# Kernel optimization log

Measured on AMD Instinct MI355X. Metric: run time of the kernel, lower is better.

## Reference

```python
import jax, jax.numpy as jnp
import numpy as np

B, T, DIM, H = 4, 2048, 512, 8
DECAY = 0.9

def setup_inputs():
    key = jax.random.key(0)
    ks = jax.random.split(key, 8)
    s = 1.0 / np.sqrt(DIM)
    def lin(k):
        return jax.random.normal(k, (DIM, DIM), jnp.float32) * s
    return {
        "q": jax.random.normal(ks[0], (B, T, DIM), jnp.float32),
        "k": jax.random.normal(ks[1], (B, T, DIM), jnp.float32),
        "v": jax.random.normal(ks[2], (B, T, DIM), jnp.float32),
        "Wa": lin(ks[3]), "ba": jnp.zeros((DIM,), jnp.float32),
        "Wb": lin(ks[4]), "bb": jnp.zeros((DIM,), jnp.float32),
        "Wg": lin(ks[5]), "bg": jnp.zeros((DIM,), jnp.float32),
        "Wo": lin(ks[6]), "bo": jnp.zeros((DIM,), jnp.float32),
    }

def _linear_scan(a, b):
    # h_t = a_t * h_{t-1} + b_t along time axis=1, via associative scan
    def combine(c1, c2):
        a1, b1 = c1
        a2, b2 = c2
        return a1 * a2, a2 * b1 + b2
    return jax.lax.associative_scan(combine, (a, b), axis=1)[1]

def reference(q, k, v, Wa, ba, Wb, bb, Wg, bg, Wo, bo):
    # --- Mamba-style selective scan on q (no residual) ---
    a = jax.nn.sigmoid(q @ Wa + ba)   # input-dependent decay [B,T,D]
    b = q @ Wb + bb                   # input injection       [B,T,D]
    h = _linear_scan(a, b)            # recurrent state       [B,T,D]
    g = jax.nn.sigmoid(q @ Wg + bg)   # gate
    m_out = (h * g) @ Wo + bo         # [B,T,D]

    # --- RetNet-style decay-weighted linear retention ---
    Dh = DIM // H
    qh = q.reshape(B, T, H, Dh)
    kh = k.reshape(B, T, H, Dh)
    vh = v.reshape(B, T, H, Dh)
    t = jnp.arange(T)
    delta = t[:, None] - t[None, :]           # t - s
    mask = delta >= 0                         # causal
    decay_mat = jnp.where(
        mask,
        jnp.exp(jnp.where(mask, delta, 0).astype(jnp.float32) * np.float32(np.log(DECAY))),
        0.0,
    )                                          # [T,T]
    scores = jnp.einsum('bthd,bshd->bhts', qh, kh) * decay_mat  # [B,H,T,T]
    r_out = jnp.einsum('bhts,bshd->bthd', scores, vh).reshape(B, T, DIM)

    return m_out + r_out
```

## Files before the change

kernel.cpp:

```cpp
#include <hip/hip_runtime.h>
#include <hip/hip_bf16.h>

typedef unsigned short u16;

#define BB 4
#define TT 2048
#define DIM 512
#define NH 8
#define DH 64
#define DECAY 0.9f

#define CC 64
#define NC 32
#define BHN 32

#define CHS 32
#define NSC 64

#define TM 128
#define TN 128
#define BK 64

#define SS 72

typedef __attribute__((ext_vector_type(8))) short bf16x8;
typedef __attribute__((ext_vector_type(4))) float f32x4;

__device__ __forceinline__ u16 f2bfu(float f) {
  union { float f; unsigned int u; } c; c.f = f;
  unsigned int u = c.u + 0x7FFFu + ((c.u >> 16) & 1u);
  return (u16)(u >> 16);
}
__device__ __forceinline__ float bf2f(u16 u) {
  union { unsigned int u; float f; } c; c.u = ((unsigned int)u) << 16;
  return c.f;
}

__device__ __forceinline__ void gl_lds16(const void* g, void* l) {
  __builtin_amdgcn_global_load_lds(
      (const __attribute__((address_space(1))) void*)g,
      (__attribute__((address_space(3))) void*)(unsigned int)(unsigned long long)l,
      16, 0, 0);
}

__device__ __forceinline__ void gemm_tile(
    int nTile, int mTile, const u16* __restrict__ A, const u16* __restrict__ Bt,
    const float* __restrict__ b0, const float* __restrict__ b1,
    const float* __restrict__ b2,
    u16* __restrict__ C0, u16* __restrict__ C1, u16* __restrict__ C2,
    int act_mask, u16* As, u16* Bs, int tid) {
  int wave = tid >> 6, lane = tid & 63;
  int group = (nTile * TN) >> 9;
  const float* bias = (group == 0) ? b0 : (group == 1) ? b1 : b2;
  u16* C = (group == 0) ? C0 : (group == 1) ? C1 : C2;
  int act = (act_mask >> group) & 1;

  int wm = (wave >> 1) * 64, wn = (wave & 1) * 64;
  int rowA = lane & 15, khalf = lane >> 4;

  f32x4 acc[4][4];
#pragma unroll
  for (int i = 0; i < 4; ++i)
#pragma unroll
    for (int j = 0; j < 4; ++j) acc[i][j] = (f32x4){0.f, 0.f, 0.f, 0.f};

  const u16* Abase = A + (size_t)mTile * TM * 512;
  const u16* Bbase = Bt + (size_t)nTile * TN * 512;

  for (int kk = 0; kk < 512; kk += BK) {
#pragma unroll
    for (int i = 0; i < 4; ++i) {
      int o = (wave * 4 + i) * 64 + lane;
      int row = o >> 3, gk = (o & 7) ^ (row & 7);
      gl_lds16(Abase + (size_t)row * 512 + kk + gk * 8, &As[o * 8]);
    }
#pragma unroll
    for (int i = 0; i < 4; ++i) {
      int o = (wave * 4 + i) * 64 + lane;
      int row = o >> 3, gk = (o & 7) ^ (row & 7);
      gl_lds16(Bbase + (size_t)row * 512 + kk + gk * 8, &Bs[o * 8]);
    }
    __syncthreads();
#pragma unroll
    for (int k0 = 0; k0 < 2; ++k0) {
      bf16x8 af[4], bfr[4];
#pragma unroll
      for (int mi = 0; mi < 4; ++mi) {
        int rr = wm + mi * 16 + rowA;
        int gk = k0 * 4 + khalf;
        int o = rr * 8 + (gk ^ (rr & 7));
        af[mi] = *(const bf16x8*)&As[o * 8];
      }
#pragma unroll
      for (int ni = 0; ni < 4; ++ni) {
        int rr = wn + ni * 16 + rowA;
        int gk = k0 * 4 + khalf;
        int o = rr * 8 + (gk ^ (rr & 7));
        bfr[ni] = *(const bf16x8*)&Bs[o * 8];
      }
#pragma unroll
      for (int mi = 0; mi < 4; ++mi)
#pragma unroll
        for (int ni = 0; ni < 4; ++ni)
          acc[mi][ni] = __builtin_amdgcn_mfma_f32_16x16x32_bf16(
              af[mi], bfr[ni], acc[mi][ni], 0, 0, 0);
    }
    __syncthreads();
  }
  int cloc = lane & 15, rq = (lane >> 4) * 4;
#pragma unroll
  for (int mi = 0; mi < 4; ++mi) {
#pragma unroll
    for (int r = 0; r < 4; ++r) {
      int m = mTile * TM + wm + mi * 16 + rq + r;
#pragma unroll
      for (int ni = 0; ni < 4; ++ni) {
        int n = (nTile * TN + wn + ni * 16 + cloc) & 511;
        float vv = acc[mi][ni][r] + bias[n];
        if (act) vv = 1.0f / (1.0f + __expf(-vv));
        C[(size_t)m * 512 + n] = f2bfu(vv);
      }
    }
  }
}

__device__ __forceinline__ void gemm_tile64(
    int nTile, int mTile, const u16* __restrict__ A, const u16* __restrict__ Bt,
    const float* __restrict__ bias, float* __restrict__ C,
    const u16* __restrict__ Radd, u16* As, u16* Bs, int tid) {
  int wave = tid >> 6, lane = tid & 63;
  int wm = wave * 32;
  int rowA = lane & 15, khalf = lane >> 4;

  f32x4 acc[2][4];
#pragma unroll
  for (int i = 0; i < 2; ++i)
#pragma unroll
    for (int j = 0; j < 4; ++j) acc[i][j] = (f32x4){0.f, 0.f, 0.f, 0.f};

  const u16* Abase = A + (size_t)mTile * TM * 512;
  const u16* Bbase = Bt + (size_t)nTile * 64 * 512;

  for (int kk = 0; kk < 512; kk += BK) {
#pragma unroll
    for (int i = 0; i < 4; ++i) {
      int o = (wave * 4 + i) * 64 + lane;
      int row = o >> 3, gk = (o & 7) ^ (row & 7);
      gl_lds16(Abase + (size_t)row * 512 + kk + gk * 8, &As[o * 8]);
    }
#pragma unroll
    for (int i = 0; i < 2; ++i) {
      int o = (wave * 2 + i) * 64 + lane;
      int row = o >> 3, gk = (o & 7) ^ (row & 7);
      gl_lds16(Bbase + (size_t)row * 512 + kk + gk * 8, &Bs[o * 8]);
    }
    __syncthreads();
#pragma unroll
    for (int k0 = 0; k0 < 2; ++k0) {
      bf16x8 af[2], bfr[4];
#pragma unroll
      for (int mi = 0; mi < 2; ++mi) {
        int rr = wm + mi * 16 + rowA;
        int gk = k0 * 4 + khalf;
        int o = rr * 8 + (gk ^ (rr & 7));
        af[mi] = *(const bf16x8*)&As[o * 8];
      }
#pragma unroll
      for (int ni = 0; ni < 4; ++ni) {
        int rr = ni * 16 + rowA;
        int gk = k0 * 4 + khalf;
        int o = rr * 8 + (gk ^ (rr & 7));
        bfr[ni] = *(const bf16x8*)&Bs[o * 8];
      }
#pragma unroll
      for (int mi = 0; mi < 2; ++mi)
#pragma unroll
        for (int ni = 0; ni < 4; ++ni)
          acc[mi][ni] = __builtin_amdgcn_mfma_f32_16x16x32_bf16(
              af[mi], bfr[ni], acc[mi][ni], 0, 0, 0);
    }
    __syncthreads();
  }
  int cloc = lane & 15, rq = (lane >> 4) * 4;
#pragma unroll
  for (int mi = 0; mi < 2; ++mi) {
#pragma unroll
    for (int r = 0; r < 4; ++r) {
      int m = mTile * TM + wm + mi * 16 + rq + r;
#pragma unroll
      for (int ni = 0; ni < 4; ++ni) {
        int n = nTile * 64 + ni * 16 + cloc;
        float vv = acc[mi][ni][r] + bias[n] + bf2f(Radd[(size_t)m * 512 + n]);
        C[(size_t)m * 512 + n] = vv;
      }
    }
  }
}

__device__ __forceinline__ void dev_retscan(int unit, int tid,
    const u16* __restrict__ KVTb, u16* __restrict__ Ptb) {
  int gid = unit * 256 + tid;
  int bh = gid >> 12, ed = gid & 4095;
  float carry = 0.f;
  const float dC = __powf(DECAY, (float)CC);
#pragma unroll
  for (int c = 0; c < NC; ++c) {
    size_t idx = ((size_t)(c * BHN + bh)) * 4096 + ed;
    Ptb[idx] = f2bfu(carry);
    carry = fmaf(dC, carry, bf2f(KVTb[idx]));
  }
}

__device__ __forceinline__ void dev_part(int unit, int tid,
    const u16* __restrict__ Ab16, const u16* __restrict__ Bb16,
    float2* __restrict__ SAB) {
  int ci = unit >> 3, grp = unit & 7;
  int ch = grp * 256 + tid;
  int bb2 = ch >> 9, d = ch & 511;
  size_t base = ((size_t)bb2 * TT + ci * CHS) * DIM + d;
  float h = 0.f, pA = 1.f;
#pragma unroll
  for (int t = 0; t < CHS; ++t) {
    float av = bf2f(Ab16[base + (size_t)t * DIM]);
    float bv = bf2f(Bb16[base + (size_t)t * DIM]);
    h = fmaf(av, h, bv);
    pA *= av;
  }
  SAB[(size_t)ci * 2048 + ch] = make_float2(pA, h);
}

__device__ __forceinline__ void dev_apply(int unit, int tid,
    const u16* __restrict__ Ab16, const u16* __restrict__ Bb16,
    const u16* __restrict__ g, const float2* __restrict__ SAB,
    u16* __restrict__ hg) {
  int ci = unit >> 3, grp = unit & 7;
  int ch = grp * 256 + tid;
  int bb = ch >> 9, d = ch & 511;
  float carry = 0.f;
  int p = 0;
  for (; p + 8 <= ci; p += 8) {
    float2 s[8];
#pragma unroll
    for (int j = 0; j < 8; ++j) s[j] = SAB[(size_t)(p + j) * 2048 + ch];
#pragma unroll
    for (int j = 0; j < 8; ++j) carry = fmaf(s[j].x, carry, s[j].y);
  }
  for (; p < ci; ++p) {
    float2 s = SAB[(size_t)p * 2048 + ch];
    carry = fmaf(s.x, carry, s.y);
  }
  size_t base = ((size_t)bb * TT + ci * CHS) * DIM + d;
  float h = carry;
#pragma unroll
  for (int t = 0; t < CHS; ++t) {
    size_t idx = base + (size_t)t * DIM;
    h = fmaf(bf2f(Ab16[idx]), h, bf2f(Bb16[idx]));
    hg[idx] = f2bfu(h * bf2f(g[idx]));
  }
}

__device__ __forceinline__ void dev_retout(int unit, int tid,
    u16* Sa, float* dp, float* dpi,
    const u16* __restrict__ qbf, const u16* __restrict__ kcb,
    const u16* __restrict__ VTg, const u16* __restrict__ Ptb,
    u16* __restrict__ routb) {
  int bh = unit & 31, c = unit >> 5;
  int b = bh >> 3, h = bh & 7;
  int wave = tid >> 6, lane = tid & 63;
  size_t base = ((size_t)(b * TT + c * CC)) * DIM + h * DH;
  if (tid < 66) dp[tid] = __powf(DECAY, (float)tid);
  if (tid < 64) dpi[tid] = __powf(DECAY, (float)tid - 63.0f);

  int wm = (wave >> 1) * 32, wn = (wave & 1) * 32;
  int rowA = lane & 15, khalf = lane >> 4;

  bf16x8 afq[2][2];
#pragma unroll
  for (int k0 = 0; k0 < 2; ++k0)
#pragma unroll
    for (int mi = 0; mi < 2; ++mi)
      afq[k0][mi] = *(const bf16x8*)(qbf + base +
          (size_t)(wm + mi * 16 + rowA) * 512 + (k0 * 4 + khalf) * 8);
  const u16* kcbase = kcb + ((size_t)bh * NC + c) * 64 * 64;
  bf16x8 bfk[2][2];
#pragma unroll
  for (int k0 = 0; k0 < 2; ++k0)
#pragma unroll
    for (int ni = 0; ni < 2; ++ni)
      bfk[k0][ni] = *(const bf16x8*)(kcbase +
          (size_t)(wn + ni * 16 + rowA) * 64 + (k0 * 4 + khalf) * 8);

  f32x4 accS[2][2];
#pragma unroll
  for (int i = 0; i < 2; ++i)
#pragma unroll
    for (int j = 0; j < 2; ++j) accS[i][j] = (f32x4){0.f, 0.f, 0.f, 0.f};
#pragma unroll
  for (int k0 = 0; k0 < 2; ++k0)
#pragma unroll
    for (int mi = 0; mi < 2; ++mi)
#pragma unroll
      for (int ni = 0; ni < 2; ++ni)
        accS[mi][ni] = __builtin_amdgcn_mfma_f32_16x16x32_bf16(
            afq[k0][mi], bfk[k0][ni], accS[mi][ni], 0, 0, 0);
  __syncthreads();

  int cloc = lane & 15, rq = (lane >> 4) * 4;
#pragma unroll
  for (int mi = 0; mi < 2; ++mi)
#pragma unroll
    for (int ni = 0; ni < 2; ++ni)
#pragma unroll
      for (int r = 0; r < 4; ++r) {
        int i = wm + mi * 16 + rq + r;
        int j = wn + ni * 16 + cloc;
        float sv = (j <= i) ? accS[mi][ni][r] * dpi[i] : 0.f;
        Sa[i * SS + j] = f2bfu(sv);
      }
#pragma unroll
  for (int mi = 0; mi < 2; ++mi) {
    float s = dp[wm + mi * 16 + rowA + 1];
#pragma unroll
    for (int k0 = 0; k0 < 2; ++k0) {
      bf16x8 t = afq[k0][mi];
#pragma unroll
      for (int u = 0; u < 8; ++u)
        t[u] = (short)f2bfu(bf2f((u16)t[u]) * s);
      afq[k0][mi] = t;
    }
  }
  __syncthreads();

  f32x4 accO[2][2];
#pragma unroll
  for (int i = 0; i < 2; ++i)
#pragma unroll
    for (int j = 0; j < 2; ++j) accO[i][j] = (f32x4){0.f, 0.f, 0.f, 0.f};
#pragma unroll
  for (int k0 = 0; k0 < 4; ++k0) {
    bf16x8 af[2], bfv[2];
#pragma unroll
    for (int mi = 0; mi < 2; ++mi) {
      if (k0 < 2)
        af[mi] = *(const bf16x8*)&Sa[(wm + mi * 16 + rowA) * SS +
                                     (k0 * 4 + khalf) * 8];
      else
        af[mi] = afq[k0 - 2][mi];
    }
#pragma unroll
    for (int ni = 0; ni < 2; ++ni) {
      int e = wn + ni * 16 + rowA;
      if (k0 < 2)
        bfv[ni] = *(const bf16x8*)(VTg + ((size_t)bh * 64 + e) * TT + c * 64 +
                                   (k0 * 4 + khalf) * 8);
      else
        bfv[ni] = *(const bf16x8*)(Ptb + ((size_t)(c * BHN + bh)) * 4096 +
                                   e * 64 + ((k0 - 2) * 4 + khalf) * 8);
    }
#pragma unroll
    for (int mi = 0; mi < 2; ++mi)
#pragma unroll
      for (int ni = 0; ni < 2; ++ni)
        accO[mi][ni] = __builtin_amdgcn_mfma_f32_16x16x32_bf16(
            af[mi], bfv[ni], accO[mi][ni], 0, 0, 0);
  }
#pragma unroll
  for (int mi = 0; mi < 2; ++mi)
#pragma unroll
    for (int r = 0; r < 4; ++r) {
      int i = wm + mi * 16 + rq + r;
#pragma unroll
      for (int ni = 0; ni < 2; ++ni) {
        int e = wn + ni * 16 + cloc;
        routb[base + (size_t)i * 512 + e] = f2bfu(accO[mi][ni][r]);
      }
    }
}

__global__ __launch_bounds__(256) void k1_prep_retkv(
    const float* __restrict__ q, u16* __restrict__ qbf,
    const float* __restrict__ W0, const float* __restrict__ W1,
    const float* __restrict__ W2, const float* __restrict__ W3,
    u16* __restrict__ Wt,
    const float* __restrict__ k, const float* __restrict__ v,
    u16* __restrict__ KVTb, u16* __restrict__ VTg, u16* __restrict__ kcb) {
  __shared__ __align__(16) u16 smem[2 * 64 * SS];
  __shared__ float t[32][33];
  int bx = blockIdx.x, tid = threadIdx.x;
  if (bx < 1024) {
    int bh = bx & 31, c = bx >> 5;
    int b = bh >> 3, h = bh & 7;
    int wave = tid >> 6, lane = tid & 63;
    u16* VT = smem;
    u16* KT = smem + 64 * SS;
    size_t base = ((size_t)(b * TT + c * CC)) * DIM + h * DH;
    int row = tid >> 2, part = tid & 3, e0 = part * 16;
    float w = __powf(DECAY, (float)(63 - row));
    __align__(16) u16 krow[16];
    {
      const float4* vs = (const float4*)(v + base + (size_t)row * DIM + e0);
      const float4* ks = (const float4*)(k + base + (size_t)row * DIM + e0);
#pragma unroll
      for (int u4 = 0; u4 < 4; ++u4) {
        float4 fv = vs[u4], fk = ks[u4];
        VT[(e0 + u4 * 4 + 0) * SS + row] = f2bfu(fv.x);
        VT[(e0 + u4 * 4 + 1) * SS + row] = f2bfu(fv.y);
        VT[(e0 + u4 * 4 + 2) * SS + row] = f2bfu(fv.z);
        VT[(e0 + u4 * 4 + 3) * SS + row] = f2bfu(fv.w);
        u16 k0s = f2bfu(fk.x * w), k1s = f2bfu(fk.y * w);
        u16 k2s = f2bfu(fk.z * w), k3s = f2bfu(fk.w * w);
        KT[(e0 + u4 * 4 + 0) * SS + row] = k0s;
        KT[(e0 + u4 * 4 + 1) * SS + row] = k1s;
        KT[(e0 + u4 * 4 + 2) * SS + row] = k2s;
        KT[(e0 + u4 * 4 + 3) * SS + row] = k3s;
        krow[u4 * 4 + 0] = k0s; krow[u4 * 4 + 1] = k1s;
        krow[u4 * 4 + 2] = k2s; krow[u4 * 4 + 3] = k3s;
      }
    }
    {
      u16* kdst = kcb + (((size_t)bh * NC + c) * 64 + row) * 64 + e0;
      *(uint4*)kdst = *(const uint4*)&krow[0];
      *(uint4*)(kdst + 8) = *(const uint4*)&krow[8];
    }
    __syncthreads();
    {
      int e = row;
      u16* dst = VTg + ((size_t)bh * 64 + e) * TT + c * 64 + part * 16;
      *(uint4*)dst = *(const uint4*)&VT[e * SS + part * 16];
      *(uint4*)(dst + 8) = *(const uint4*)&VT[e * SS + part * 16 + 8];
    }
    int wm = (wave >> 1) * 32, wn = (wave & 1) * 32;
    int rowA = lane & 15, khalf = lane >> 4;
    f32x4 acc[2][2];
#pragma unroll
    for (int i = 0; i < 2; ++i)
#pragma unroll
      for (int j = 0; j < 2; ++j) acc[i][j] = (f32x4){0.f, 0.f, 0.f, 0.f};
#pragma unroll
    for (int k0 = 0; k0 < 2; ++k0) {
      int gk = k0 * 4 + khalf;
      bf16x8 af[2], bfr[2];
#pragma unroll
      for (int mi = 0; mi < 2; ++mi)
        af[mi] = *(const bf16x8*)&VT[(wm + mi * 16 + rowA) * SS + gk * 8];
#pragma unroll
      for (int ni = 0; ni < 2; ++ni)
        bfr[ni] = *(const bf16x8*)&KT[(wn + ni * 16 + rowA) * SS + gk * 8];
#pragma unroll
      for (int mi = 0; mi < 2; ++mi)
#pragma unroll
        for (int ni = 0; ni < 2; ++ni)
          acc[mi][ni] = __builtin_amdgcn_mfma_f32_16x16x32_bf16(
              af[mi], bfr[ni], acc[mi][ni], 0, 0, 0);
    }
    int cloc = lane & 15, rq = (lane >> 4) * 4;
    u16* o = KVTb + ((size_t)(c * BHN + bh)) * 4096;
#pragma unroll
    for (int mi = 0; mi < 2; ++mi)
#pragma unroll
      for (int r = 0; r < 4; ++r) {
        int e = wm + mi * 16 + rq + r;
#pragma unroll
        for (int ni = 0; ni < 2; ++ni)
          o[e * 64 + (wn + ni * 16 + cloc)] = f2bfu(acc[mi][ni][r]);
      }
  } else if (bx < 2048) {
    int bx2 = bx - 1024;
    int m = bx2 >> 8, rem = bx2 & 255;
    int n0 = (rem & 15) * 32, k0 = (rem >> 4) * 32;
    const float* W = (m == 0) ? W0 : (m == 1) ? W1 : (m == 2) ? W2 : W3;
    int tx = tid & 31, ty = tid >> 5;
#pragma unroll
    for (int r = 0; r < 32; r += 8)
      t[ty + r][tx] = W[(size_t)(k0 + ty + r) * DIM + n0 + tx];
    __syncthreads();
    u16* o = Wt + (size_t)m * DIM * DIM;
#pragma unroll
    for (int r = 0; r < 32; r += 8)
      o[(size_t)(n0 + ty + r) * DIM + k0 + tx] = f2bfu(t[tx][ty + r]);
  } else {
    int i0 = ((bx - 2048) * 256 + tid) * 2;
#pragma unroll
    for (int u2 = 0; u2 < 2; ++u2) {
      float4 f = ((const float4*)q)[i0 + u2];
      ushort4 u;
      u.x = f2bfu(f.x); u.y = f2bfu(f.y); u.z = f2bfu(f.z); u.w = f2bfu(f.w);
      ((ushort4*)qbf)[i0 + u2] = u;
    }
  }
}

__global__ __launch_bounds__(256) void k2_gemm1_retscan(
    const u16* __restrict__ qbf, const u16* __restrict__ WtAll,
    const float* __restrict__ ba, const float* __restrict__ bb,
    const float* __restrict__ bg,
    u16* __restrict__ Ab16, u16* __restrict__ Bb16, u16* __restrict__ Gb16,
    const u16* __restrict__ KVTb, u16* __restrict__ Ptb) {
  __shared__ __align__(16) u16 smem[TM * BK + TN * BK];
  int bx = blockIdx.x, tid = threadIdx.x;
  if (bx < 768) {
    int r = bx & 7, t6 = bx >> 3;
    int nT = t6 % 12, s = t6 / 12;
    int mT = (s << 3) | r;
    gemm_tile(nT, mT, qbf, WtAll, ba, bb, bg, Ab16, Bb16, Gb16,
              0b101, smem, smem + TM * BK, tid);
  } else {
    dev_retscan(bx - 768, tid, KVTb, Ptb);
  }
}

__global__ __launch_bounds__(256) void k3_retout_part(
    const u16* __restrict__ Ab16, const u16* __restrict__ Bb16,
    float2* __restrict__ SAB,
    const u16* __restrict__ qbf, const u16* __restrict__ kcb,
    const u16* __restrict__ VTg, const u16* __restrict__ Ptb,
    u16* __restrict__ routb) {
  __shared__ __align__(16) u16 Sa[64 * SS];
  __shared__ float dp[66];
  __shared__ float dpi[64];
  int bx = blockIdx.x, tid = threadIdx.x;
  if (bx >= 512) {
    dev_part(bx - 512, tid, Ab16, Bb16, SAB);
    return;
  }
  dev_retout(bx, tid, Sa, dp, dpi, qbf, kcb, VTg, Ptb, routb);
}

__global__ __launch_bounds__(256) void k4_apply_retout(
    const u16* __restrict__ Ab16, const u16* __restrict__ Bb16,
    const u16* __restrict__ g, const float2* __restrict__ SAB,
    u16* __restrict__ hg,
    const u16* __restrict__ qbf, const u16* __restrict__ kcb,
    const u16* __restrict__ VTg, const u16* __restrict__ Ptb,
    u16* __restrict__ routb) {
  __shared__ __align__(16) u16 Sa[64 * SS];
  __shared__ float dp[66];
  __shared__ float dpi[64];
  int bx = blockIdx.x, tid = threadIdx.x;
  if (bx < 512) {
    dev_apply(511 - bx, tid, Ab16, Bb16, g, SAB, hg);
    return;
  }
  dev_retout(bx, tid, Sa, dp, dpi, qbf, kcb, VTg, Ptb, routb);
}

__global__ __launch_bounds__(256) void k5_gemm2(
    const u16* __restrict__ hgbf, const u16* __restrict__ Wto,
    const float* __restrict__ bo, float* __restrict__ out,
    const u16* __restrict__ routb) {
  __shared__ __align__(16) u16 smem[TM * BK + 64 * BK];
  int bx = blockIdx.x;
  int r = bx & 7, t6 = bx >> 3;
  int nT = t6 & 7, s = t6 >> 3;
  int mT = (s << 3) | r;
  gemm_tile64(nT, mT, hgbf, Wto, bo, out, routb,
              smem, smem + TM * BK, threadIdx.x);
}

extern "C" void kernel_launch(void* const* d_in, const int* in_sizes, int n_in,
                              void* d_out, int out_size, void* d_ws, size_t ws_size,
                              hipStream_t stream) {
  const float* q  = (const float*)d_in[0];
  const float* k  = (const float*)d_in[1];
  const float* v  = (const float*)d_in[2];
  const float* Wa = (const float*)d_in[3];
  const float* ba = (const float*)d_in[4];
  const float* Wb = (const float*)d_in[5];
  const float* bb = (const float*)d_in[6];
  const float* Wg = (const float*)d_in[7];
  const float* bg = (const float*)d_in[8];
  const float* Wo = (const float*)d_in[9];
  const float* bo = (const float*)d_in[10];
  float* out = (float*)d_out;

  const size_t NEL = (size_t)BB * TT * DIM;
  float2* SAB = (float2*)d_ws;
  u16* up = (u16*)(SAB + (size_t)NSC * 2048);
  u16* Ab16  = up;  up += NEL;
  u16* Bb16  = up;  up += NEL;
  u16* Gb16  = up;  up += NEL;
  u16* qbf   = up;  up += NEL;
  u16* hgbf  = up;  up += NEL;
  u16* WtAll = up;  up += 4 * DIM * DIM;
  u16* KVTb  = up;  up += (size_t)NC * BHN * 4096;
  u16* Ptb   = up;  up += (size_t)NC * BHN * 4096;
  u16* VTg   = up;  up += (size_t)BHN * 64 * TT;
  u16* routb = up;  up += NEL;
  u16* kcb   = up;  up += (size_t)BHN * NC * 64 * 64;

  k1_prep_retkv<<<4096, 256, 0, stream>>>(q, qbf, Wa, Wb, Wg, Wo, WtAll,
                                          k, v, KVTb, VTg, kcb);

  k2_gemm1_retscan<<<1280, 256, 0, stream>>>(qbf, WtAll, ba, bb, bg,
                                             Ab16, Bb16, Gb16, KVTb, Ptb);

  k3_retout_part<<<1024, 256, 0, stream>>>(Ab16, Bb16, SAB,
                                           qbf, kcb, VTg, Ptb, routb);

  k4_apply_retout<<<1024, 256, 0, stream>>>(Ab16, Bb16, Gb16, SAB, hgbf,
                                            qbf, kcb, VTg, Ptb, routb);

  k5_gemm2<<<512, 256, 0, stream>>>(hgbf, WtAll + 3 * DIM * DIM,
                                    bo, out, routb);
}
```

Measured before the change: 164.2 us.

## Fuse chunk-summary scan into a/b GEMM epilogue and merge retention-output passes

The a and b projections are now computed together in one tile with two accumulator sets, and the epilogue computes each 32-step chunk's product-of-decays and partial state directly from registers using cross-lane shuffles. This removes the separate pass that reread Ab16/Bb16 to build SAB. It also collapses the two half-launches of retention output into a single kernel, so one launch is dropped. In exchange the fused tile doubles accumulator registers and LDS use, which may lower occupancy.

```diff
diff --git a/kernel.cpp b/kernel.cpp
--- a/kernel.cpp
+++ b/kernel.cpp
@@ -43,29 +43,28 @@
       16, 0, 0);
 }
 
-__device__ __forceinline__ void gemm_tile(
-    int nTile, int mTile, const u16* __restrict__ A, const u16* __restrict__ Bt,
-    const float* __restrict__ b0, const float* __restrict__ b1,
-    const float* __restrict__ b2,
-    u16* __restrict__ C0, u16* __restrict__ C1, u16* __restrict__ C2,
-    int act_mask, u16* As, u16* Bs, int tid) {
+__device__ __forceinline__ void gemm_tile_ab(
+    int nTile, int mTile, const u16* __restrict__ A,
+    const u16* __restrict__ Wta, const u16* __restrict__ Wtb,
+    const float* __restrict__ ba, const float* __restrict__ bb,
+    u16* __restrict__ Ca, u16* __restrict__ Cb, float2* __restrict__ SAB,
+    u16* As, u16* Bsa, u16* Bsb, int tid) {
   int wave = tid >> 6, lane = tid & 63;
-  int group = (nTile * TN) >> 9;
-  const float* bias = (group == 0) ? b0 : (group == 1) ? b1 : b2;
-  u16* C = (group == 0) ? C0 : (group == 1) ? C1 : C2;
-  int act = (act_mask >> group) & 1;
-
   int wm = (wave >> 1) * 64, wn = (wave & 1) * 64;
   int rowA = lane & 15, khalf = lane >> 4;
 
-  f32x4 acc[4][4];
+  f32x4 acca[4][4], accb[4][4];
 #pragma unroll
   for (int i = 0; i < 4; ++i)
 #pragma unroll
-    for (int j = 0; j < 4; ++j) acc[i][j] = (f32x4){0.f, 0.f, 0.f, 0.f};
+    for (int j = 0; j < 4; ++j) {
+      acca[i][j] = (f32x4){0.f, 0.f, 0.f, 0.f};
+      accb[i][j] = (f32x4){0.f, 0.f, 0.f, 0.f};
+    }
 
   const u16* Abase = A + (size_t)mTile * TM * 512;
-  const u16* Bbase = Bt + (size_t)nTile * TN * 512;
+  const u16* BabB = Wta + (size_t)nTile * TN * 512;
+  const u16* BbbB = Wtb + (size_t)nTile * TN * 512;
 
   for (int kk = 0; kk < 512; kk += BK) {
 #pragma unroll
@@ -78,12 +77,18 @@
     for (int i = 0; i < 4; ++i) {
       int o = (wave * 4 + i) * 64 + lane;
       int row = o >> 3, gk = (o & 7) ^ (row & 7);
-      gl_lds16(Bbase + (size_t)row * 512 + kk + gk * 8, &Bs[o * 8]);
+      gl_lds16(BabB + (size_t)row * 512 + kk + gk * 8, &Bsa[o * 8]);
+    }
+#pragma unroll
+    for (int i = 0; i < 4; ++i) {
+      int o = (wave * 4 + i) * 64 + lane;
+      int row = o >> 3, gk = (o & 7) ^ (row & 7);
+      gl_lds16(BbbB + (size_t)row * 512 + kk + gk * 8, &Bsb[o * 8]);
     }
     __syncthreads();
 #pragma unroll
     for (int k0 = 0; k0 < 2; ++k0) {
-      bf16x8 af[4], bfr[4];
+      bf16x8 af[4], bfa[4], bfb[4];
 #pragma unroll
       for (int mi = 0; mi < 4; ++mi) {
         int rr = wm + mi * 16 + rowA;
@@ -96,6 +101,114 @@
         int rr = wn + ni * 16 + rowA;
         int gk = k0 * 4 + khalf;
         int o = rr * 8 + (gk ^ (rr & 7));
+        bfa[ni] = *(const bf16x8*)&Bsa[o * 8];
+        bfb[ni] = *(const bf16x8*)&Bsb[o * 8];
+      }
+#pragma unroll
+      for (int mi = 0; mi < 4; ++mi)
+#pragma unroll
+        for (int ni = 0; ni < 4; ++ni) {
+          acca[mi][ni] = __builtin_amdgcn_mfma_f32_16x16x32_bf16(
+              af[mi], bfa[ni], acca[mi][ni], 0, 0, 0);
+          accb[mi][ni] = __builtin_amdgcn_mfma_f32_16x16x32_bf16(
+              af[mi], bfb[ni], accb[mi][ni], 0, 0, 0);
+        }
+    }
+    __syncthreads();
+  }
+  int cloc = lane & 15, q = lane >> 4, rq = q * 4;
+#pragma unroll
+  for (int chunk = 0; chunk < 2; ++chunk) {
+#pragma unroll
+    for (int ni = 0; ni < 4; ++ni) {
+      int n = nTile * TN + wn + ni * 16 + cloc;
+      float pa0 = 1.f, h0 = 0.f, pa1 = 1.f, h1 = 0.f;
+#pragma unroll
+      for (int half = 0; half < 2; ++half) {
+        int mi = chunk * 2 + half;
+#pragma unroll
+        for (int r = 0; r < 4; ++r) {
+          int m = mTile * TM + wm + mi * 16 + rq + r;
+          float av = 1.0f / (1.0f + __expf(-(acca[mi][ni][r] + ba[n])));
+          float bv = accb[mi][ni][r] + bb[n];
+          u16 ua = f2bfu(av), ub = f2bfu(bv);
+          Ca[(size_t)m * 512 + n] = ua;
+          Cb[(size_t)m * 512 + n] = ub;
+          float avr = bf2f(ua), bvr = bf2f(ub);
+          if (half == 0) { h0 = fmaf(avr, h0, bvr); pa0 *= avr; }
+          else           { h1 = fmaf(avr, h1, bvr); pa1 *= avr; }
+        }
+      }
+      float pas[8], hs[8];
+#pragma unroll
+      for (int j = 0; j < 4; ++j) {
+        int src = cloc + j * 16;
+        pas[j] = __shfl(pa0, src);
+        hs[j] = __shfl(h0, src);
+        pas[4 + j] = __shfl(pa1, src);
+        hs[4 + j] = __shfl(h1, src);
+      }
+      float paT = pas[0], hT = hs[0];
+#pragma unroll
+      for (int s = 1; s < 8; ++s) {
+        hT = fmaf(pas[s], hT, hs[s]);
+        paT *= pas[s];
+      }
+      if (q == 0) {
+        int g_ci = mTile * 4 + (wave >> 1) * 2 + chunk;
+        SAB[(size_t)(g_ci & 63) * 2048 + (g_ci >> 6) * 512 + n] =
+            make_float2(paT, hT);
+      }
+    }
+  }
+}
+
+__device__ __forceinline__ void gemm_tile_g(
+    int nTile, int mTile, const u16* __restrict__ A, const u16* __restrict__ Bt,
+    const float* __restrict__ bias, u16* __restrict__ C,
+    u16* As, u16* Bs, int tid) {
+  int wave = tid >> 6, lane = tid & 63;
+  int wm = (wave >> 1) * 64, wn = (wave & 1) * 64;
+  int rowA = lane & 15, khalf = lane >> 4;
+
+  f32x4 acc[4][4];
+#pragma unroll
+  for (int i = 0; i < 4; ++i)
+#pragma unroll
+    for (int j = 0; j < 4; ++j) acc[i][j] = (f32x4){0.f, 0.f, 0.f, 0.f};
+
+  const u16* Abase = A + (size_t)mTile * TM * 512;
+  const u16* Bbase = Bt + (size_t)nTile * TN * 512;
+
+  for (int kk = 0; kk < 512; kk += BK) {
+#pragma unroll
+    for (int i = 0; i < 4; ++i) {
+      int o = (wave * 4 + i) * 64 + lane;
+      int row = o >> 3, gk = (o & 7) ^ (row & 7);
+      gl_lds16(Abase + (size_t)row * 512 + kk + gk * 8, &As[o * 8]);
+    }
+#pragma unroll
+    for (int i = 0; i < 4; ++i) {
+      int o = (wave * 4 + i) * 64 + lane;
+      int row = o >> 3, gk = (o & 7) ^ (row & 7);
+      gl_lds16(Bbase + (size_t)row * 512 + kk + gk * 8, &Bs[o * 8]);
+    }
+    __syncthreads();
+#pragma unroll
+    for (int k0 = 0; k0 < 2; ++k0) {
+      bf16x8 af[4], bfr[4];
+#pragma unroll
+      for (int mi = 0; mi < 4; ++mi) {
+        int rr = wm + mi * 16 + rowA;
+        int gk = k0 * 4 + khalf;
+        int o = rr * 8 + (gk ^ (rr & 7));
+        af[mi] = *(const bf16x8*)&As[o * 8];
+      }
+#pragma unroll
+      for (int ni = 0; ni < 4; ++ni) {
+        int rr = wn + ni * 16 + rowA;
+        int gk = k0 * 4 + khalf;
+        int o = rr * 8 + (gk ^ (rr & 7));
         bfr[ni] = *(const bf16x8*)&Bs[o * 8];
       }
 #pragma unroll
@@ -115,9 +228,9 @@
       int m = mTile * TM + wm + mi * 16 + rq + r;
 #pragma unroll
       for (int ni = 0; ni < 4; ++ni) {
-        int n = (nTile * TN + wn + ni * 16 + cloc) & 511;
+        int n = nTile * TN + wn + ni * 16 + cloc;
         float vv = acc[mi][ni][r] + bias[n];
-        if (act) vv = 1.0f / (1.0f + __expf(-vv));
+        vv = 1.0f / (1.0f + __expf(-vv));
         C[(size_t)m * 512 + n] = f2bfu(vv);
       }
     }
@@ -209,24 +322,6 @@
     Ptb[idx] = f2bfu(carry);
     carry = fmaf(dC, carry, bf2f(KVTb[idx]));
   }
-}
-
-__device__ __forceinline__ void dev_part(int unit, int tid,
-    const u16* __restrict__ Ab16, const u16* __restrict__ Bb16,
-    float2* __restrict__ SAB) {
-  int ci = unit >> 3, grp = unit & 7;
-  int ch = grp * 256 + tid;
-  int bb2 = ch >> 9, d = ch & 511;
-  size_t base = ((size_t)bb2 * TT + ci * CHS) * DIM + d;
-  float h = 0.f, pA = 1.f;
-#pragma unroll
-  for (int t = 0; t < CHS; ++t) {
-    float av = bf2f(Ab16[base + (size_t)t * DIM]);
-    float bv = bf2f(Bb16[base + (size_t)t * DIM]);
-    h = fmaf(av, h, bv);
-    pA *= av;
-  }
-  SAB[(size_t)ci * 2048 + ch] = make_float2(pA, h);
 }
 
 __device__ __forceinline__ void dev_apply(int unit, int tid,
@@ -495,38 +590,30 @@
     const float* __restrict__ ba, const float* __restrict__ bb,
     const float* __restrict__ bg,
     u16* __restrict__ Ab16, u16* __restrict__ Bb16, u16* __restrict__ Gb16,
+    float2* __restrict__ SAB,
     const u16* __restrict__ KVTb, u16* __restrict__ Ptb) {
-  __shared__ __align__(16) u16 smem[TM * BK + TN * BK];
+  __shared__ __align__(16) u16 smem[3 * TM * BK];
   int bx = blockIdx.x, tid = threadIdx.x;
-  if (bx < 768) {
+  if (bx < 256) {
     int r = bx & 7, t6 = bx >> 3;
-    int nT = t6 % 12, s = t6 / 12;
+    int nT = t6 & 3, s = t6 >> 2;
     int mT = (s << 3) | r;
-    gemm_tile(nT, mT, qbf, WtAll, ba, bb, bg, Ab16, Bb16, Gb16,
-              0b101, smem, smem + TM * BK, tid);
+    gemm_tile_ab(nT, mT, qbf, WtAll, WtAll + 512 * 512, ba, bb,
+                 Ab16, Bb16, SAB, smem, smem + TM * BK, smem + 2 * TM * BK,
+                 tid);
+  } else if (bx < 512) {
+    int bx2 = bx - 256;
+    int r = bx2 & 7, t6 = bx2 >> 3;
+    int nT = t6 & 3, s = t6 >> 2;
+    int mT = (s << 3) | r;
+    gemm_tile_g(nT, mT, qbf, WtAll + 2 * 512 * 512, bg, Gb16,
+                smem, smem + TM * BK, tid);
   } else {
-    dev_retscan(bx - 768, tid, KVTb, Ptb);
-  }
-}
-
-__global__ __launch_bounds__(256) void k3_retout_part(
-    const u16* __restrict__ Ab16, const u16* __restrict__ Bb16,
-    float2* __restrict__ SAB,
-    const u16* __restrict__ qbf, const u16* __restrict__ kcb,
-    const u16* __restrict__ VTg, const u16* __restrict__ Ptb,
-    u16* __restrict__ routb) {
-  __shared__ __align__(16) u16 Sa[64 * SS];
-  __shared__ float dp[66];
-  __shared__ float dpi[64];
-  int bx = blockIdx.x, tid = threadIdx.x;
-  if (bx >= 512) {
-    dev_part(bx - 512, tid, Ab16, Bb16, SAB);
-    return;
-  }
-  dev_retout(bx, tid, Sa, dp, dpi, qbf, kcb, VTg, Ptb, routb);
-}
-
-__global__ __launch_bounds__(256) void k4_apply_retout(
+    dev_retscan(bx - 512, tid, KVTb, Ptb);
+  }
+}
+
+__global__ __launch_bounds__(256) void k3_apply_retout(
     const u16* __restrict__ Ab16, const u16* __restrict__ Bb16,
     const u16* __restrict__ g, const float2* __restrict__ SAB,
     u16* __restrict__ hg,
@@ -541,10 +628,10 @@
     dev_apply(511 - bx, tid, Ab16, Bb16, g, SAB, hg);
     return;
   }
-  dev_retout(bx, tid, Sa, dp, dpi, qbf, kcb, VTg, Ptb, routb);
-}
-
-__global__ __launch_bounds__(256) void k5_gemm2(
+  dev_retout(bx - 512, tid, Sa, dp, dpi, qbf, kcb, VTg, Ptb, routb);
+}
+
+__global__ __launch_bounds__(256) void k4_gemm2(
     const u16* __restrict__ hgbf, const u16* __restrict__ Wto,
     const float* __restrict__ bo, float* __restrict__ out,
     const u16* __restrict__ routb) {
@@ -591,15 +678,13 @@
   k1_prep_retkv<<<4096, 256, 0, stream>>>(q, qbf, Wa, Wb, Wg, Wo, WtAll,
                                           k, v, KVTb, VTg, kcb);
 
-  k2_gemm1_retscan<<<1280, 256, 0, stream>>>(qbf, WtAll, ba, bb, bg,
-                                             Ab16, Bb16, Gb16, KVTb, Ptb);
-
-  k3_retout_part<<<1024, 256, 0, stream>>>(Ab16, Bb16, SAB,
-                                           qbf, kcb, VTg, Ptb, routb);
-
-  k4_apply_retout<<<1024, 256, 0, stream>>>(Ab16, Bb16, Gb16, SAB, hgbf,
+  k2_gemm1_retscan<<<1024, 256, 0, stream>>>(qbf, WtAll, ba, bb, bg,
+                                             Ab16, Bb16, Gb16, SAB,
+                                             KVTb, Ptb);
+
+  k3_apply_retout<<<1536, 256, 0, stream>>>(Ab16, Bb16, Gb16, SAB, hgbf,
                                             qbf, kcb, VTg, Ptb, routb);
 
-  k5_gemm2<<<512, 256, 0, stream>>>(hgbf, WtAll + 3 * DIM * DIM,
+  k4_gemm2<<<512, 256, 0, stream>>>(hgbf, WtAll + 3 * DIM * DIM,
                                     bo, out, routb);
 }
```

Result: slower. 174.7 us (+6.4%).

## Rebalance retention stages across kernels to co-schedule with GEMM and scan work

Applied to the files above, without the earlier changes.

Moves the retention K/V chunk prep (KV outer products, transposed V, scaled K) from the prep kernel into the first GEMM kernel. The retention scan is paired with the scan partials kernel, and all retention output blocks are merged into the apply kernel. The number of launches stays the same, but work is regrouped so heterogeneous block types run side by side and each kernel's tail shrinks. Retout blocks that previously ran in the partial-scan kernel now all share one launch with apply, which may make that kernel longer.

```diff
diff --git a/kernel.cpp b/kernel.cpp
--- a/kernel.cpp
+++ b/kernel.cpp
@@ -377,96 +377,15 @@
     }
 }
 
-__global__ __launch_bounds__(256) void k1_prep_retkv(
+__global__ __launch_bounds__(256) void k0_prep(
     const float* __restrict__ q, u16* __restrict__ qbf,
     const float* __restrict__ W0, const float* __restrict__ W1,
     const float* __restrict__ W2, const float* __restrict__ W3,
-    u16* __restrict__ Wt,
-    const float* __restrict__ k, const float* __restrict__ v,
-    u16* __restrict__ KVTb, u16* __restrict__ VTg, u16* __restrict__ kcb) {
-  __shared__ __align__(16) u16 smem[2 * 64 * SS];
+    u16* __restrict__ Wt) {
   __shared__ float t[32][33];
   int bx = blockIdx.x, tid = threadIdx.x;
   if (bx < 1024) {
-    int bh = bx & 31, c = bx >> 5;
-    int b = bh >> 3, h = bh & 7;
-    int wave = tid >> 6, lane = tid & 63;
-    u16* VT = smem;
-    u16* KT = smem + 64 * SS;
-    size_t base = ((size_t)(b * TT + c * CC)) * DIM + h * DH;
-    int row = tid >> 2, part = tid & 3, e0 = part * 16;
-    float w = __powf(DECAY, (float)(63 - row));
-    __align__(16) u16 krow[16];
-    {
-      const float4* vs = (const float4*)(v + base + (size_t)row * DIM + e0);
-      const float4* ks = (const float4*)(k + base + (size_t)row * DIM + e0);
-#pragma unroll
-      for (int u4 = 0; u4 < 4; ++u4) {
-        float4 fv = vs[u4], fk = ks[u4];
-        VT[(e0 + u4 * 4 + 0) * SS + row] = f2bfu(fv.x);
-        VT[(e0 + u4 * 4 + 1) * SS + row] = f2bfu(fv.y);
-        VT[(e0 + u4 * 4 + 2) * SS + row] = f2bfu(fv.z);
-        VT[(e0 + u4 * 4 + 3) * SS + row] = f2bfu(fv.w);
-        u16 k0s = f2bfu(fk.x * w), k1s = f2bfu(fk.y * w);
-        u16 k2s = f2bfu(fk.z * w), k3s = f2bfu(fk.w * w);
-        KT[(e0 + u4 * 4 + 0) * SS + row] = k0s;
-        KT[(e0 + u4 * 4 + 1) * SS + row] = k1s;
-        KT[(e0 + u4 * 4 + 2) * SS + row] = k2s;
-        KT[(e0 + u4 * 4 + 3) * SS + row] = k3s;
-        krow[u4 * 4 + 0] = k0s; krow[u4 * 4 + 1] = k1s;
-        krow[u4 * 4 + 2] = k2s; krow[u4 * 4 + 3] = k3s;
-      }
-    }
-    {
-      u16* kdst = kcb + (((size_t)bh * NC + c) * 64 + row) * 64 + e0;
-      *(uint4*)kdst = *(const uint4*)&krow[0];
-      *(uint4*)(kdst + 8) = *(const uint4*)&krow[8];
-    }
-    __syncthreads();
-    {
-      int e = row;
-      u16* dst = VTg + ((size_t)bh * 64 + e) * TT + c * 64 + part * 16;
-      *(uint4*)dst = *(const uint4*)&VT[e * SS + part * 16];
-      *(uint4*)(dst + 8) = *(const uint4*)&VT[e * SS + part * 16 + 8];
-    }
-    int wm = (wave >> 1) * 32, wn = (wave & 1) * 32;
-    int rowA = lane & 15, khalf = lane >> 4;
-    f32x4 acc[2][2];
-#pragma unroll
-    for (int i = 0; i < 2; ++i)
-#pragma unroll
-      for (int j = 0; j < 2; ++j) acc[i][j] = (f32x4){0.f, 0.f, 0.f, 0.f};
-#pragma unroll
-    for (int k0 = 0; k0 < 2; ++k0) {
-      int gk = k0 * 4 + khalf;
-      bf16x8 af[2], bfr[2];
-#pragma unroll
-      for (int mi = 0; mi < 2; ++mi)
-        af[mi] = *(const bf16x8*)&VT[(wm + mi * 16 + rowA) * SS + gk * 8];
-#pragma unroll
-      for (int ni = 0; ni < 2; ++ni)
-        bfr[ni] = *(const bf16x8*)&KT[(wn + ni * 16 + rowA) * SS + gk * 8];
-#pragma unroll
-      for (int mi = 0; mi < 2; ++mi)
-#pragma unroll
-        for (int ni = 0; ni < 2; ++ni)
-          acc[mi][ni] = __builtin_amdgcn_mfma_f32_16x16x32_bf16(
-              af[mi], bfr[ni], acc[mi][ni], 0, 0, 0);
-    }
-    int cloc = lane & 15, rq = (lane >> 4) * 4;
-    u16* o = KVTb + ((size_t)(c * BHN + bh)) * 4096;
-#pragma unroll
-    for (int mi = 0; mi < 2; ++mi)
-#pragma unroll
-      for (int r = 0; r < 4; ++r) {
-        int e = wm + mi * 16 + rq + r;
-#pragma unroll
-        for (int ni = 0; ni < 2; ++ni)
-          o[e * 64 + (wn + ni * 16 + cloc)] = f2bfu(acc[mi][ni][r]);
-      }
-  } else if (bx < 2048) {
-    int bx2 = bx - 1024;
-    int m = bx2 >> 8, rem = bx2 & 255;
+    int m = bx >> 8, rem = bx & 255;
     int n0 = (rem & 15) * 32, k0 = (rem >> 4) * 32;
     const float* W = (m == 0) ? W0 : (m == 1) ? W1 : (m == 2) ? W2 : W3;
     int tx = tid & 31, ty = tid >> 5;
@@ -479,7 +398,7 @@
     for (int r = 0; r < 32; r += 8)
       o[(size_t)(n0 + ty + r) * DIM + k0 + tx] = f2bfu(t[tx][ty + r]);
   } else {
-    int i0 = ((bx - 2048) * 256 + tid) * 2;
+    int i0 = ((bx - 1024) * 256 + tid) * 2;
 #pragma unroll
     for (int u2 = 0; u2 < 2; ++u2) {
       float4 f = ((const float4*)q)[i0 + u2];
@@ -490,12 +409,13 @@
   }
 }
 
-__global__ __launch_bounds__(256) void k2_gemm1_retscan(
+__global__ __launch_bounds__(256) void k1_gemm1_retkv(
     const u16* __restrict__ qbf, const u16* __restrict__ WtAll,
     const float* __restrict__ ba, const float* __restrict__ bb,
     const float* __restrict__ bg,
     u16* __restrict__ Ab16, u16* __restrict__ Bb16, u16* __restrict__ Gb16,
-    const u16* __restrict__ KVTb, u16* __restrict__ Ptb) {
+    const float* __restrict__ k, const float* __restrict__ v,
+    u16* __restrict__ KVTb, u16* __restrict__ VTg, u16* __restrict__ kcb) {
   __shared__ __align__(16) u16 smem[TM * BK + TN * BK];
   int bx = blockIdx.x, tid = threadIdx.x;
   if (bx < 768) {
@@ -504,29 +424,100 @@
     int mT = (s << 3) | r;
     gemm_tile(nT, mT, qbf, WtAll, ba, bb, bg, Ab16, Bb16, Gb16,
               0b101, smem, smem + TM * BK, tid);
-  } else {
-    dev_retscan(bx - 768, tid, KVTb, Ptb);
-  }
-}
-
-__global__ __launch_bounds__(256) void k3_retout_part(
+    return;
+  }
+  int bx2 = bx - 768;
+  int bh = bx2 & 31, c = bx2 >> 5;
+  int b = bh >> 3, h = bh & 7;
+  int wave = tid >> 6, lane = tid & 63;
+  u16* VT = smem;
+  u16* KT = smem + 64 * SS;
+  size_t base = ((size_t)(b * TT + c * CC)) * DIM + h * DH;
+  int row = tid >> 2, part = tid & 3, e0 = part * 16;
+  float w = __powf(DECAY, (float)(63 - row));
+  __align__(16) u16 krow[16];
+  {
+    const float4* vs = (const float4*)(v + base + (size_t)row * DIM + e0);
+    const float4* ks = (const float4*)(k + base + (size_t)row * DIM + e0);
+#pragma unroll
+    for (int u4 = 0; u4 < 4; ++u4) {
+      float4 fv = vs[u4], fk = ks[u4];
+      VT[(e0 + u4 * 4 + 0) * SS + row] = f2bfu(fv.x);
+      VT[(e0 + u4 * 4 + 1) * SS + row] = f2bfu(fv.y);
+      VT[(e0 + u4 * 4 + 2) * SS + row] = f2bfu(fv.z);
+      VT[(e0 + u4 * 4 + 3) * SS + row] = f2bfu(fv.w);
+      u16 k0s = f2bfu(fk.x * w), k1s = f2bfu(fk.y * w);
+      u16 k2s = f2bfu(fk.z * w), k3s = f2bfu(fk.w * w);
+      KT[(e0 + u4 * 4 + 0) * SS + row] = k0s;
+      KT[(e0 + u4 * 4 + 1) * SS + row] = k1s;
+      KT[(e0 + u4 * 4 + 2) * SS + row] = k2s;
+      KT[(e0 + u4 * 4 + 3) * SS + row] = k3s;
+      krow[u4 * 4 + 0] = k0s; krow[u4 * 4 + 1] = k1s;
+      krow[u4 * 4 + 2] = k2s; krow[u4 * 4 + 3] = k3s;
+    }
+  }
+  {
+    u16* kdst = kcb + (((size_t)bh * NC + c) * 64 + row) * 64 + e0;
+    *(uint4*)kdst = *(const uint4*)&krow[0];
+    *(uint4*)(kdst + 8) = *(const uint4*)&krow[8];
+  }
+  __syncthreads();
+  {
+    int e = row;
+    u16* dst = VTg + ((size_t)bh * 64 + e) * TT + c * 64 + part * 16;
+    *(uint4*)dst = *(const uint4*)&VT[e * SS + part * 16];
+    *(uint4*)(dst + 8) = *(const uint4*)&VT[e * SS + part * 16 + 8];
+  }
+  int wm = (wave >> 1) * 32, wn = (wave & 1) * 32;
+  int rowA = lane & 15, khalf = lane >> 4;
+  f32x4 acc[2][2];
+#pragma unroll
+  for (int i = 0; i < 2; ++i)
+#pragma unroll
+    for (int j = 0; j < 2; ++j) acc[i][j] = (f32x4){0.f, 0.f, 0.f, 0.f};
+#pragma unroll
+  for (int k0 = 0; k0 < 2; ++k0) {
+    int gk = k0 * 4 + khalf;
+    bf16x8 af[2], bfr[2];
+#pragma unroll
+    for (int mi = 0; mi < 2; ++mi)
+      af[mi] = *(const bf16x8*)&VT[(wm + mi * 16 + rowA) * SS + gk * 8];
+#pragma unroll
+    for (int ni = 0; ni < 2; ++ni)
+      bfr[ni] = *(const bf16x8*)&KT[(wn + ni * 16 + rowA) * SS + gk * 8];
+#pragma unroll
+    for (int mi = 0; mi < 2; ++mi)
+#pragma unroll
+      for (int ni = 0; ni < 2; ++ni)
+        acc[mi][ni] = __builtin_amdgcn_mfma_f32_16x16x32_bf16(
+            af[mi], bfr[ni], acc[mi][ni], 0, 0, 0);
+  }
+  int cloc = lane & 15, rq = (lane >> 4) * 4;
+  u16* o = KVTb + ((size_t)(c * BHN + bh)) * 4096;
+#pragma unroll
+  for (int mi = 0; mi < 2; ++mi)
+#pragma unroll
+    for (int r = 0; r < 4; ++r) {
+      int e = wm + mi * 16 + rq + r;
+#pragma unroll
+      for (int ni = 0; ni < 2; ++ni)
+        o[e * 64 + (wn + ni * 16 + cloc)] = f2bfu(acc[mi][ni][r]);
+    }
+}
+
+__global__ __launch_bounds__(256) void k2_retscan_part(
+    const u16* __restrict__ KVTb, u16* __restrict__ Ptb,
     const u16* __restrict__ Ab16, const u16* __restrict__ Bb16,
-    float2* __restrict__ SAB,
-    const u16* __restrict__ qbf, const u16* __restrict__ kcb,
-    const u16* __restrict__ VTg, const u16* __restrict__ Ptb,
-    u16* __restrict__ routb) {
-  __shared__ __align__(16) u16 Sa[64 * SS];
-  __shared__ float dp[66];
-  __shared__ float dpi[64];
+    float2* __restrict__ SAB) {
   int bx = blockIdx.x, tid = threadIdx.x;
-  if (bx >= 512) {
-    dev_part(bx - 512, tid, Ab16, Bb16, SAB);
+  if (bx < 512) {
+    dev_retscan(bx, tid, KVTb, Ptb);
     return;
   }
-  dev_retout(bx, tid, Sa, dp, dpi, qbf, kcb, VTg, Ptb, routb);
-}
-
-__global__ __launch_bounds__(256) void k4_apply_retout(
+  dev_part(bx - 512, tid, Ab16, Bb16, SAB);
+}
+
+__global__ __launch_bounds__(256) void k3_apply_retout(
     const u16* __restrict__ Ab16, const u16* __restrict__ Bb16,
     const u16* __restrict__ g, const float2* __restrict__ SAB,
     u16* __restrict__ hg,
@@ -541,10 +532,10 @@
     dev_apply(511 - bx, tid, Ab16, Bb16, g, SAB, hg);
     return;
   }
-  dev_retout(bx, tid, Sa, dp, dpi, qbf, kcb, VTg, Ptb, routb);
-}
-
-__global__ __launch_bounds__(256) void k5_gemm2(
+  dev_retout(bx - 512, tid, Sa, dp, dpi, qbf, kcb, VTg, Ptb, routb);
+}
+
+__global__ __launch_bounds__(256) void k4_gemm2(
     const u16* __restrict__ hgbf, const u16* __restrict__ Wto,
     const float* __restrict__ bo, float* __restrict__ out,
     const u16* __restrict__ routb) {
@@ -588,18 +579,17 @@
   u16* routb = up;  up += NEL;
   u16* kcb   = up;  up += (size_t)BHN * NC * 64 * 64;
 
-  k1_prep_retkv<<<4096, 256, 0, stream>>>(q, qbf, Wa, Wb, Wg, Wo, WtAll,
-                                          k, v, KVTb, VTg, kcb);
-
-  k2_gemm1_retscan<<<1280, 256, 0, stream>>>(qbf, WtAll, ba, bb, bg,
-                                             Ab16, Bb16, Gb16, KVTb, Ptb);
-
-  k3_retout_part<<<1024, 256, 0, stream>>>(Ab16, Bb16, SAB,
-                                           qbf, kcb, VTg, Ptb, routb);
-
-  k4_apply_retout<<<1024, 256, 0, stream>>>(Ab16, Bb16, Gb16, SAB, hgbf,
+  k0_prep<<<3072, 256, 0, stream>>>(q, qbf, Wa, Wb, Wg, Wo, WtAll);
+
+  k1_gemm1_retkv<<<1792, 256, 0, stream>>>(qbf, WtAll, ba, bb, bg,
+                                           Ab16, Bb16, Gb16,
+                                           k, v, KVTb, VTg, kcb);
+
+  k2_retscan_part<<<1024, 256, 0, stream>>>(KVTb, Ptb, Ab16, Bb16, SAB);
+
+  k3_apply_retout<<<1536, 256, 0, stream>>>(Ab16, Bb16, Gb16, SAB, hgbf,
                                             qbf, kcb, VTg, Ptb, routb);
 
-  k5_gemm2<<<512, 256, 0, stream>>>(hgbf, WtAll + 3 * DIM * DIM,
+  k4_gemm2<<<512, 256, 0, stream>>>(hgbf, WtAll + 3 * DIM * DIM,
                                     bo, out, routb);
 }
```

After: 163.3 us. Within noise of the previous version (-0.6%).
